# Performance work log

Measured on AMD Instinct MI355X. Metric: run time of the kernel, lower is better.

Reference implementation:

```python
import jax, jax.numpy as jnp
import numpy as np

INSTANCE_INDICES = (1, 3, 5, 7)
BOUNDARY_WEIGHT = 5.0
EROSION_ITERS = 2


def _erode_once(m):
    # scipy.ndimage.binary_erosion with default 6-connected cross structure
    # (generate_binary_structure(3,1)) and border_value=0: a voxel survives
    # iff it and all 6 face-neighbors are 1 (neighbors outside the volume are 0).
    # m: [B, K, D, H, W] float in {0,1}
    p = jnp.pad(m, ((0, 0), (0, 0), (1, 1), (1, 1), (1, 1)))
    return (m
            * p[:, :, :-2, 1:-1, 1:-1] * p[:, :, 2:, 1:-1, 1:-1]
            * p[:, :, 1:-1, :-2, 1:-1] * p[:, :, 1:-1, 2:, 1:-1]
            * p[:, :, 1:-1, 1:-1, :-2] * p[:, :, 1:-1, 1:-1, 2:])


def _bce_with_logits(logits, targets):
    # numerically stable elementwise BCE-with-logits, reduction='none'
    return jnp.maximum(logits, 0.0) - logits * targets + jnp.log1p(jnp.exp(-jnp.abs(logits)))


def setup_inputs() -> dict:
    key = jax.random.key(0)
    k1, k2, k3, k4 = jax.random.split(key, 4)
    B, C, D, H, W = 2, 8, 128, 128, 128
    logits = jax.random.normal(k1, (B, C, D, H, W), dtype=jnp.float32)
    targets = jax.random.randint(k2, (B, C, D, H, W), 0, 2).astype(jnp.float32)
    mask = jax.random.randint(k3, (B, C), 0, 2).astype(bool)
    spatial_mask = jax.random.randint(k4, (B, 1, D, H, W), 0, 2).astype(jnp.float32)
    return {"logits": logits, "targets": targets, "mask": mask, "spatial_mask": spatial_mask}


def reference(logits, targets, mask, spatial_mask):
    idx = np.array(INSTANCE_INDICES)
    inst_logits = logits[:, idx]      # [B, n_inst, D, H, W]
    inst_targets = targets[:, idx]    # [B, n_inst, D, H, W]
    inst_mask = mask[:, idx]          # [B, n_inst]

    # boundary = original - eroded (erosion_iterations applications)
    eroded = inst_targets
    for _ in range(EROSION_ITERS):
        eroded = _erode_once(eroded)
    boundaries = inst_targets - eroded

    bce = _bce_with_logits(inst_logits, inst_targets)
    bce = bce * (1.0 + (BOUNDARY_WEIGHT - 1.0) * boundaries)

    # combine per-class mask [B,n_inst] with spatial mask [B,1,D,H,W]
    combined = inst_mask.astype(jnp.float32)[:, :, None, None, None] * spatial_mask
    bce = bce * combined

    n_voxels = combined.sum()
    return jnp.where(n_voxels > 0, bce.sum() / jnp.maximum(n_voxels, 1.0), 0.0)
```

## Files before the change

kernel.cpp:

```cpp
#include <hip/hip_runtime.h>


#define DD 128
#define HH 128
#define WW 128
#define HW_ (HH * WW)
#define DHW (DD * HH * WW)

typedef unsigned long long ull;

#define PK_BYTE_OFF 32768
#define NSLOT 1024

__global__ void __launch_bounds__(256) bal_pack(const float* __restrict__ targets,
                                                const int*   __restrict__ mask,
                                                ull*         __restrict__ pk)
{
    const int ch = blockIdx.y;
    const int b  = ch >> 2;
    const int c  = (ch & 3) * 2 + 1;
    if (mask[b * 8 + c] == 0) return;

    const int tid = threadIdx.x;
    const size_t blockbase = (size_t)blockIdx.x * 8192;
    const float* tg  = targets + (size_t)(b * 8 + c) * DHW + blockbase;
    ull*         pko = pk + (size_t)ch * 32768 + (blockbase >> 6);

    #pragma unroll
    for (int k = 0; k < 8; ++k) {
        float4 t4 = *(const float4*)(tg + k * 1024 + tid * 4);
        unsigned nib = (unsigned)(t4.x > 0.5f)
                     | ((unsigned)(t4.y > 0.5f) << 1)
                     | ((unsigned)(t4.z > 0.5f) << 2)
                     | ((unsigned)(t4.w > 0.5f) << 3);
        ull v = ((ull)nib) << ((tid & 15) * 4);
        v |= __shfl_xor(v, 1);
        v |= __shfl_xor(v, 2);
        v |= __shfl_xor(v, 4);
        v |= __shfl_xor(v, 8);
        if ((tid & 15) == 0)
            pko[k * 16 + (tid >> 4)] = v;
    }
}

__global__ void __launch_bounds__(256) bal_main(const float* __restrict__ logits,
                                                const float* __restrict__ spatial,
                                                const int*   __restrict__ mask,
                                                const ull*   __restrict__ pk,
                                                double*      __restrict__ pr)
{
    const int b   = blockIdx.y;
    const int bx  = blockIdx.x;
    const int z   = bx >> 2;
    const int y0  = (bx & 3) * 32;
    const int tid = threadIdx.x;
    const int wave = tid >> 6;
    const int lane = tid & 63;
    const int sid  = b * 512 + bx;

    const int m0 = mask[b * 8 + 1], m1 = mask[b * 8 + 3];
    const int m2 = mask[b * 8 + 5], m3 = mask[b * 8 + 7];
    if ((m0 | m1 | m2 | m3) == 0) {
        if (tid == 0) { pr[2 * sid] = 0.0; pr[2 * sid + 1] = 0.0; }
        return;
    }

    __shared__ ull   tile[4][5][36][3];
    __shared__ float sp[4096];
    __shared__ float sb[4], sn[4];

    for (int idx = tid; idx < 1440; idx += 256) {
        const int ch  = idx / 360;
        int rem       = idx - ch * 360;
        const int dz  = rem / 72;
        rem          -= dz * 72;
        const int rowl = rem >> 1;
        const int h    = rem & 1;
        const int zz = z + dz - 2;
        const int yy = y0 + rowl - 2;
        ull v = 0ull;
        if (((unsigned)zz < 128u) & ((unsigned)yy < 128u))
            v = pk[(size_t)(b * 4 + ch) * 32768 + (size_t)(((zz << 7) + yy) << 1) + h];
        tile[ch][dz][rowl][h] = v;
    }
    const int gbase = z * HW_ + y0 * WW;
    const float* spg = spatial + (size_t)b * DHW + gbase;
    #pragma unroll
    for (int k = 0; k < 4; ++k) {
        const int f = (tid + k * 256) * 4;
        *(float4*)(sp + f) = *(const float4*)(spg + f);
    }
    __syncthreads();

    const int act = (wave == 0) ? m0 : (wave == 1) ? m1 : (wave == 2) ? m2 : m3;

    float acc = 0.0f, n = 0.0f;
    if (act) {
        const int rl = (lane >> 1) + 2;
        const int h  = lane & 1;
        ull c0 = tile[wave][2][rl][0];
        ull c1 = tile[wave][2][rl][1];
        ull elo = c0 & ((c0 >> 1) | (c1 << 63)) & (c0 << 1)
                     & ((c0 >> 2) | (c1 << 62)) & (c0 << 2);
        ull ehi = c1 & (c1 >> 1) & ((c1 << 1) | (c0 >> 63))
                     & (c1 >> 2) & ((c1 << 2) | (c0 >> 62));
        {
            ull a0, a1;
            a0 = tile[wave][1][rl][0]; a1 = tile[wave][1][rl][1];
            elo &= a0 & ((a0 >> 1) | (a1 << 63)) & (a0 << 1);
            ehi &= a1 & (a1 >> 1) & ((a1 << 1) | (a0 >> 63));
            a0 = tile[wave][3][rl][0]; a1 = tile[wave][3][rl][1];
            elo &= a0 & ((a0 >> 1) | (a1 << 63)) & (a0 << 1);
            ehi &= a1 & (a1 >> 1) & ((a1 << 1) | (a0 >> 63));
            a0 = tile[wave][2][rl - 1][0]; a1 = tile[wave][2][rl - 1][1];
            elo &= a0 & ((a0 >> 1) | (a1 << 63)) & (a0 << 1);
            ehi &= a1 & (a1 >> 1) & ((a1 << 1) | (a0 >> 63));
            a0 = tile[wave][2][rl + 1][0]; a1 = tile[wave][2][rl + 1][1];
            elo &= a0 & ((a0 >> 1) | (a1 << 63)) & (a0 << 1);
            ehi &= a1 & (a1 >> 1) & ((a1 << 1) | (a0 >> 63));
        }
        {
            ull a0, a1;
            a0 = tile[wave][0][rl][0];     a1 = tile[wave][0][rl][1];     elo &= a0; ehi &= a1;
            a0 = tile[wave][4][rl][0];     a1 = tile[wave][4][rl][1];     elo &= a0; ehi &= a1;
            a0 = tile[wave][2][rl - 2][0]; a1 = tile[wave][2][rl - 2][1]; elo &= a0; ehi &= a1;
            a0 = tile[wave][2][rl + 2][0]; a1 = tile[wave][2][rl + 2][1]; elo &= a0; ehi &= a1;
            a0 = tile[wave][1][rl - 1][0]; a1 = tile[wave][1][rl - 1][1]; elo &= a0; ehi &= a1;
            a0 = tile[wave][1][rl + 1][0]; a1 = tile[wave][1][rl + 1][1]; elo &= a0; ehi &= a1;
            a0 = tile[wave][3][rl - 1][0]; a1 = tile[wave][3][rl - 1][1]; elo &= a0; ehi &= a1;
            a0 = tile[wave][3][rl + 1][0]; a1 = tile[wave][3][rl + 1][1]; elo &= a0; ehi &= a1;
        }
        const ull ero   = h ? ehi : elo;
        const ull tbits = h ? c1  : c0;

        const int c = wave * 2 + 1;
        const float* lg = logits + (size_t)(b * 8 + c) * DHW + gbase;

        #pragma unroll 4
        for (int m = 0; m < 16; ++m) {
            const int q   = 4 * m + (lane >> 4);
            const ull er  = __shfl(ero, q);
            const ull tb  = __shfl(tbits, q);
            const int sh  = (lane & 15) * 4;
            const unsigned eb  = (unsigned)(er >> sh) & 0xFu;
            const unsigned tbn = (unsigned)(tb >> sh) & 0xFu;
            const int voff = q * 64 + sh;
            const float4 l4 = *(const float4*)(lg + voff);
            const float4 s4 = *(const float4*)(sp + voff);
            #define PROC(LV, SV, TB, EB)                                              \
            {                                                                         \
                const float tf = (float)(TB);                                         \
                const float w  = fmaf(4.0f, tf - (float)(EB), 1.0f);                  \
                const float a  = fabsf(LV);                                           \
                const float u  = __builtin_amdgcn_exp2f(a * -1.4426950408889634f);    \
                const float so = __builtin_amdgcn_logf(1.0f + u) * 0.6931471805599453f;\
                const float bce = fmaxf(LV, 0.0f) - (LV) * tf + so;                   \
                acc = fmaf((SV) * w, bce, acc);                                       \
                n += (SV);                                                            \
            }
            PROC(l4.x, s4.x, tbn & 1u,        eb & 1u)
            PROC(l4.y, s4.y, (tbn >> 1) & 1u, (eb >> 1) & 1u)
            PROC(l4.z, s4.z, (tbn >> 2) & 1u, (eb >> 2) & 1u)
            PROC(l4.w, s4.w, (tbn >> 3) & 1u, (eb >> 3) & 1u)
            #undef PROC
        }
    }

    #pragma unroll
    for (int o = 32; o > 0; o >>= 1) {
        acc += __shfl_down(acc, o);
        n   += __shfl_down(n, o);
    }
    if (lane == 0) { sb[wave] = acc; sn[wave] = n; }
    __syncthreads();
    if (tid == 0) {
        pr[2 * sid]     = (double)(sb[0] + sb[1] + sb[2] + sb[3]);
        pr[2 * sid + 1] = (double)(sn[0] + sn[1] + sn[2] + sn[3]);
    }
}

__global__ void __launch_bounds__(256) bal_finalize(const double* __restrict__ pr,
                                                    float* __restrict__ out)
{
    double s = 0.0, n = 0.0;
    for (int i = threadIdx.x; i < NSLOT; i += 256) {
        s += pr[2 * i];
        n += pr[2 * i + 1];
    }
    #pragma unroll
    for (int o = 32; o > 0; o >>= 1) {
        s += __shfl_down(s, o);
        n += __shfl_down(n, o);
    }
    __shared__ double ss[4], nn[4];
    const int wave = threadIdx.x >> 6;
    if ((threadIdx.x & 63) == 0) { ss[wave] = s; nn[wave] = n; }
    __syncthreads();
    if (threadIdx.x == 0) {
        const double S = ss[0] + ss[1] + ss[2] + ss[3];
        const double N = nn[0] + nn[1] + nn[2] + nn[3];
        out[0] = (N > 0.0) ? (float)(S / (N < 1.0 ? 1.0 : N)) : 0.0f;
    }
}

__device__ __constant__ signed char OFFS[24][3] = {
    {-1,0,0},{1,0,0},{0,-1,0},{0,1,0},{0,0,-1},{0,0,1},
    {-2,0,0},{2,0,0},{0,-2,0},{0,2,0},{0,0,-2},{0,0,2},
    {-1,-1,0},{-1,1,0},{1,-1,0},{1,1,0},
    {-1,0,-1},{-1,0,1},{1,0,-1},{1,0,1},
    {0,-1,-1},{0,-1,1},{0,1,-1},{0,1,1}
};

__global__ void __launch_bounds__(256) bal_direct(
    const float* __restrict__ logits, const float* __restrict__ targets,
    const int* __restrict__ mask, const float* __restrict__ spatial,
    double* __restrict__ ws)
{
    const int ch = blockIdx.y;
    const int b  = ch >> 2;
    const int c  = 2 * (ch & 3) + 1;
    if (mask[b * 8 + c] == 0) return;
    const float* lg = logits  + (size_t)(b * 8 + c) * DHW;
    const float* tg = targets + (size_t)(b * 8 + c) * DHW;
    const float* sp = spatial + (size_t)b * DHW;
    const int tid = threadIdx.x;
    const int row = blockIdx.x * 8 + (tid >> 5);
    const int x0  = (tid & 31) * 4;
    const int z   = row >> 7;
    const int y   = row & 127;
    const size_t off = (size_t)row * WW + x0;
    float4 s4 = *(const float4*)(sp + off);
    float n_local   = s4.x + s4.y + s4.z + s4.w;
    float bce_local = 0.0f;
    if (n_local > 0.0f) {
        float4 l4 = *(const float4*)(lg + off);
        float4 t4 = *(const float4*)(tg + off);
        const float sv[4] = {s4.x, s4.y, s4.z, s4.w};
        const float lv[4] = {l4.x, l4.y, l4.z, l4.w};
        const float tv[4] = {t4.x, t4.y, t4.z, t4.w};
        #pragma unroll
        for (int j = 0; j < 4; ++j) {
            if (sv[j] == 0.0f) continue;
            const float l = lv[j];
            const float t = tv[j];
            float bce = fmaxf(l, 0.0f) - l * t + log1pf(expf(-fabsf(l)));
            float w = 1.0f;
            if (t > 0.5f) {
                float e = 1.0f;
                const int x = x0 + j;
                for (int k = 0; k < 24; ++k) {
                    const int zz = z + OFFS[k][0];
                    const int yy = y + OFFS[k][1];
                    const int xx = x + OFFS[k][2];
                    float v = 0.0f;
                    if (((unsigned)zz < 128u) & ((unsigned)yy < 128u) & ((unsigned)xx < 128u))
                        v = tg[zz * HW_ + yy * WW + xx];
                    if (v < 0.5f) { e = 0.0f; break; }
                }
                w = 1.0f + 4.0f * (1.0f - e);
            }
            bce_local += bce * w;
        }
    }
    #pragma unroll
    for (int o = 32; o > 0; o >>= 1) {
        bce_local += __shfl_down(bce_local, o);
        n_local   += __shfl_down(n_local, o);
    }
    __shared__ float sb[4], sn[4];
    const int wave = tid >> 6;
    if ((tid & 63) == 0) { sb[wave] = bce_local; sn[wave] = n_local; }
    __syncthreads();
    if (tid == 0) {
        atomicAdd(&ws[0], (double)(sb[0] + sb[1] + sb[2] + sb[3]));
        atomicAdd(&ws[1], (double)(sn[0] + sn[1] + sn[2] + sn[3]));
    }
}

__global__ void bal_finalize_ws(const double* __restrict__ ws, float* __restrict__ out)
{
    const double s = ws[0];
    const double n = ws[1];
    out[0] = (n > 0.0) ? (float)(s / (n < 1.0 ? 1.0 : n)) : 0.0f;
}

extern "C" void kernel_launch(void* const* d_in, const int* in_sizes, int n_in,
                              void* d_out, int out_size, void* d_ws, size_t ws_size,
                              hipStream_t stream)
{
    const float* logits  = (const float*)d_in[0];
    const float* targets = (const float*)d_in[1];
    const int*   mask    = (const int*)d_in[2];
    const float* spatial = (const float*)d_in[3];

    const size_t need = PK_BYTE_OFF + (size_t)8 * 32768 * sizeof(ull);
    if (ws_size >= need) {
        ull*    pk = (ull*)((char*)d_ws + PK_BYTE_OFF);
        double* pr = (double*)d_ws;
        bal_pack<<<dim3(256, 8), 256, 0, stream>>>(targets, mask, pk);
        bal_main<<<dim3(512, 2), 256, 0, stream>>>(logits, spatial, mask, pk, pr);
        bal_finalize<<<1, 256, 0, stream>>>(pr, (float*)d_out);
    } else {
        double* ws = (double*)d_ws;
        hipMemsetAsync(d_ws, 0, 16, stream);
        bal_direct<<<dim3(2048, 8), 256, 0, stream>>>(logits, targets, mask, spatial, ws);
        bal_finalize_ws<<<1, 1, 0, stream>>>(ws, (float*)d_out);
    }
}
```

Before: 245.6 us.

## Fuse pack, main and finalize into one cooperative kernel with grid syncs

New measurement: 243.3 us. No clear change (-0.9%).

```diff
diff --git a/kernel.cpp b/kernel.cpp
--- a/kernel.cpp
+++ b/kernel.cpp
@@ -1,4 +1,5 @@
 #include <hip/hip_runtime.h>
+#include <hip/hip_cooperative_groups.h>
 
 
 #define DD 128
@@ -9,90 +10,79 @@
 
 typedef unsigned long long ull;
 
+namespace cg = cooperative_groups;
+
 #define PK_BYTE_OFF 32768
 #define NSLOT 1024
 
-__global__ void __launch_bounds__(256) bal_pack(const float* __restrict__ targets,
-                                                const int*   __restrict__ mask,
-                                                ull*         __restrict__ pk)
-{
-    const int ch = blockIdx.y;
-    const int b  = ch >> 2;
-    const int c  = (ch & 3) * 2 + 1;
-    if (mask[b * 8 + c] == 0) return;
-
-    const int tid = threadIdx.x;
-    const size_t blockbase = (size_t)blockIdx.x * 8192;
-    const float* tg  = targets + (size_t)(b * 8 + c) * DHW + blockbase;
-    ull*         pko = pk + (size_t)ch * 32768 + (blockbase >> 6);
-
-    #pragma unroll
-    for (int k = 0; k < 8; ++k) {
-        float4 t4 = *(const float4*)(tg + k * 1024 + tid * 4);
-        unsigned nib = (unsigned)(t4.x > 0.5f)
-                     | ((unsigned)(t4.y > 0.5f) << 1)
-                     | ((unsigned)(t4.z > 0.5f) << 2)
-                     | ((unsigned)(t4.w > 0.5f) << 3);
-        ull v = ((ull)nib) << ((tid & 15) * 4);
-        v |= __shfl_xor(v, 1);
-        v |= __shfl_xor(v, 2);
-        v |= __shfl_xor(v, 4);
-        v |= __shfl_xor(v, 8);
-        if ((tid & 15) == 0)
-            pko[k * 16 + (tid >> 4)] = v;
-    }
-}
-
-__global__ void __launch_bounds__(256) bal_main(const float* __restrict__ logits,
-                                                const float* __restrict__ spatial,
-                                                const int*   __restrict__ mask,
-                                                const ull*   __restrict__ pk,
-                                                double*      __restrict__ pr)
-{
-    const int b   = blockIdx.y;
-    const int bx  = blockIdx.x;
-    const int z   = bx >> 2;
-    const int y0  = (bx & 3) * 32;
-    const int tid = threadIdx.x;
+
+__device__ __forceinline__ void pack_chunk(const float* __restrict__ tg,
+                                           ull* __restrict__ pko,
+                                           int tid, int k)
+{
+    float4 t4 = *(const float4*)(tg + k * 1024 + tid * 4);
+    unsigned nib = (unsigned)(t4.x > 0.5f)
+                 | ((unsigned)(t4.y > 0.5f) << 1)
+                 | ((unsigned)(t4.z > 0.5f) << 2)
+                 | ((unsigned)(t4.w > 0.5f) << 3);
+    ull v = ((ull)nib) << ((tid & 15) * 4);
+    v |= __shfl_xor(v, 1);
+    v |= __shfl_xor(v, 2);
+    v |= __shfl_xor(v, 4);
+    v |= __shfl_xor(v, 8);
+    if ((tid & 15) == 0)
+        pko[k * 16 + (tid >> 4)] = v;
+}
+
+__device__ __forceinline__ void main_tile_body(const float* __restrict__ logits,
+                                               const float* __restrict__ spatial,
+                                               const int*   __restrict__ mask,
+                                               const ull*   __restrict__ pk,
+                                               double*      __restrict__ pr,
+                                               int b, int bx)
+{
+    const int z    = bx >> 2;
+    const int y0   = (bx & 3) * 32;
+    const int tid  = threadIdx.x;
     const int wave = tid >> 6;
     const int lane = tid & 63;
     const int sid  = b * 512 + bx;
 
     const int m0 = mask[b * 8 + 1], m1 = mask[b * 8 + 3];
     const int m2 = mask[b * 8 + 5], m3 = mask[b * 8 + 7];
-    if ((m0 | m1 | m2 | m3) == 0) {
-        if (tid == 0) { pr[2 * sid] = 0.0; pr[2 * sid + 1] = 0.0; }
-        return;
-    }
+    const int anyact = m0 | m1 | m2 | m3;
 
     __shared__ ull   tile[4][5][36][3];
     __shared__ float sp[4096];
     __shared__ float sb[4], sn[4];
 
-    for (int idx = tid; idx < 1440; idx += 256) {
-        const int ch  = idx / 360;
-        int rem       = idx - ch * 360;
-        const int dz  = rem / 72;
-        rem          -= dz * 72;
-        const int rowl = rem >> 1;
-        const int h    = rem & 1;
-        const int zz = z + dz - 2;
-        const int yy = y0 + rowl - 2;
-        ull v = 0ull;
-        if (((unsigned)zz < 128u) & ((unsigned)yy < 128u))
-            v = pk[(size_t)(b * 4 + ch) * 32768 + (size_t)(((zz << 7) + yy) << 1) + h];
-        tile[ch][dz][rowl][h] = v;
-    }
     const int gbase = z * HW_ + y0 * WW;
-    const float* spg = spatial + (size_t)b * DHW + gbase;
-    #pragma unroll
-    for (int k = 0; k < 4; ++k) {
-        const int f = (tid + k * 256) * 4;
-        *(float4*)(sp + f) = *(const float4*)(spg + f);
+
+    if (anyact) {
+        for (int idx = tid; idx < 1440; idx += 256) {
+            const int ch  = idx / 360;
+            int rem       = idx - ch * 360;
+            const int dz  = rem / 72;
+            rem          -= dz * 72;
+            const int rowl = rem >> 1;
+            const int h    = rem & 1;
+            const int zz = z + dz - 2;
+            const int yy = y0 + rowl - 2;
+            ull v = 0ull;
+            if (((unsigned)zz < 128u) & ((unsigned)yy < 128u))
+                v = pk[(size_t)(b * 4 + ch) * 32768 + (size_t)(((zz << 7) + yy) << 1) + h];
+            tile[ch][dz][rowl][h] = v;
+        }
+        const float* spg = spatial + (size_t)b * DHW + gbase;
+        #pragma unroll
+        for (int k = 0; k < 4; ++k) {
+            const int f = (tid + k * 256) * 4;
+            *(float4*)(sp + f) = *(const float4*)(spg + f);
+        }
     }
     __syncthreads();
 
-    const int act = (wave == 0) ? m0 : (wave == 1) ? m1 : (wave == 2) ? m2 : m3;
+    const int act = anyact ? ((wave == 0) ? m0 : (wave == 1) ? m1 : (wave == 2) ? m2 : m3) : 0;
 
     float acc = 0.0f, n = 0.0f;
     if (act) {
@@ -177,6 +167,85 @@
         pr[2 * sid]     = (double)(sb[0] + sb[1] + sb[2] + sb[3]);
         pr[2 * sid + 1] = (double)(sn[0] + sn[1] + sn[2] + sn[3]);
     }
+}
+
+__global__ void __launch_bounds__(256, 4) bal_fused(const float* __restrict__ logits,
+                                                    const float* __restrict__ targets,
+                                                    const float* __restrict__ spatial,
+                                                    const int*   __restrict__ mask,
+                                                    ull*         __restrict__ pk,
+                                                    double*      __restrict__ pr,
+                                                    float*       __restrict__ out)
+{
+    cg::grid_group grid = cg::this_grid();
+    const int gid = blockIdx.x;
+    const int tid = threadIdx.x;
+
+    {
+        const int ch = gid >> 7;
+        const int b  = ch >> 2;
+        const int c  = (ch & 3) * 2 + 1;
+        if (mask[b * 8 + c] != 0) {
+            const size_t blockbase = (size_t)(gid & 127) * 16384;
+            const float* tg  = targets + (size_t)(b * 8 + c) * DHW + blockbase;
+            ull*         pko = pk + (size_t)ch * 32768 + (blockbase >> 6);
+            #pragma unroll
+            for (int k = 0; k < 16; ++k)
+                pack_chunk(tg, pko, tid, k);
+        }
+    }
+    grid.sync();
+
+    main_tile_body(logits, spatial, mask, pk, pr, gid >> 9, gid & 511);
+    grid.sync();
+
+    if (gid == 0) {
+        double s = 0.0, n = 0.0;
+        for (int i = tid; i < NSLOT; i += 256) {
+            s += pr[2 * i];
+            n += pr[2 * i + 1];
+        }
+        #pragma unroll
+        for (int o = 32; o > 0; o >>= 1) {
+            s += __shfl_down(s, o);
+            n += __shfl_down(n, o);
+        }
+        __shared__ double ss[4], nn[4];
+        const int wave = tid >> 6;
+        if ((tid & 63) == 0) { ss[wave] = s; nn[wave] = n; }
+        __syncthreads();
+        if (tid == 0) {
+            const double S = ss[0] + ss[1] + ss[2] + ss[3];
+            const double N = nn[0] + nn[1] + nn[2] + nn[3];
+            out[0] = (N > 0.0) ? (float)(S / (N < 1.0 ? 1.0 : N)) : 0.0f;
+        }
+    }
+}
+
+__global__ void __launch_bounds__(256) bal_pack(const float* __restrict__ targets,
+                                                const int*   __restrict__ mask,
+                                                ull*         __restrict__ pk)
+{
+    const int ch = blockIdx.y;
+    const int b  = ch >> 2;
+    const int c  = (ch & 3) * 2 + 1;
+    if (mask[b * 8 + c] == 0) return;
+    const int tid = threadIdx.x;
+    const size_t blockbase = (size_t)blockIdx.x * 8192;
+    const float* tg  = targets + (size_t)(b * 8 + c) * DHW + blockbase;
+    ull*         pko = pk + (size_t)ch * 32768 + (blockbase >> 6);
+    #pragma unroll
+    for (int k = 0; k < 8; ++k)
+        pack_chunk(tg, pko, tid, k);
+}
+
+__global__ void __launch_bounds__(256) bal_main(const float* __restrict__ logits,
+                                                const float* __restrict__ spatial,
+                                                const int*   __restrict__ mask,
+                                                const ull*   __restrict__ pk,
+                                                double*      __restrict__ pr)
+{
+    main_tile_body(logits, spatial, mask, pk, pr, blockIdx.y, blockIdx.x);
 }
 
 __global__ void __launch_bounds__(256) bal_finalize(const double* __restrict__ pr,
@@ -292,18 +361,38 @@
     const float* targets = (const float*)d_in[1];
     const int*   mask    = (const int*)d_in[2];
     const float* spatial = (const float*)d_in[3];
+    float*       outp    = (float*)d_out;
 
     const size_t need = PK_BYTE_OFF + (size_t)8 * 32768 * sizeof(ull);
     if (ws_size >= need) {
         ull*    pk = (ull*)((char*)d_ws + PK_BYTE_OFF);
         double* pr = (double*)d_ws;
+
+        static int coop = -1;
+        if (coop < 0) {
+            int dev = 0, v = 0;
+            if (hipGetDevice(&dev) == hipSuccess &&
+                hipDeviceGetAttribute(&v, hipDeviceAttributeCooperativeLaunch, dev) == hipSuccess)
+                coop = v ? 1 : 0;
+            else
+                coop = 0;
+        }
+        if (coop) {
+            void* args[] = { (void*)&logits, (void*)&targets, (void*)&spatial,
+                             (void*)&mask, (void*)&pk, (void*)&pr, (void*)&outp };
+            hipError_t e = hipLaunchCooperativeKernel((const void*)bal_fused,
+                                                      dim3(1024), dim3(256),
+                                                      args, 0, stream);
+            if (e == hipSuccess) return;
+            coop = 0;
+        }
         bal_pack<<<dim3(256, 8), 256, 0, stream>>>(targets, mask, pk);
         bal_main<<<dim3(512, 2), 256, 0, stream>>>(logits, spatial, mask, pk, pr);
-        bal_finalize<<<1, 256, 0, stream>>>(pr, (float*)d_out);
+        bal_finalize<<<1, 256, 0, stream>>>(pr, outp);
     } else {
         double* ws = (double*)d_ws;
         hipMemsetAsync(d_ws, 0, 16, stream);
         bal_direct<<<dim3(2048, 8), 256, 0, stream>>>(logits, targets, mask, spatial, ws);
-        bal_finalize_ws<<<1, 1, 0, stream>>>(ws, (float*)d_out);
-    }
-}
+        bal_finalize_ws<<<1, 1, 0, stream>>>(ws, outp);
+    }
+}
```
